# Optimization experiments

Measured on AMD Instinct MI355X. Metric: run time of the kernel, lower is better.

Reference implementation:

```python
import jax, jax.numpy as jnp
import numpy as np

EMBED = 768
HEADS = 12
HEAD_DIM = EMBED // HEADS  # 64
NUM_CLS = 1
WIN = 16        # one-sided window radius
DIL = 4         # dilation
THETA = 10000.0
COORD_HIGH = 100000.0


def _rotate_half(x):
    # [..., x1, x2, ...] -> [..., -x2, x1, ...] over adjacent pairs
    x1 = x[..., 0::2]
    x2 = x[..., 1::2]
    return jnp.stack([-x2, x1], axis=-1).reshape(x.shape)


def _rope2d(x, coords):
    # x: (B, H, L, head_dim); coords: (B, L, 2) pixel coords
    half = HEAD_DIM // 2
    inv_freq = 1.0 / THETA ** (jnp.arange(0, half, 2, dtype=jnp.float32) / half)  # (half/2,)
    xy = coords.astype(jnp.float32) / COORD_HIGH
    fx = xy[..., 0:1] * inv_freq  # (B, L, half/2)
    fy = xy[..., 1:2] * inv_freq
    fx = jnp.repeat(fx, 2, axis=-1)  # (B, L, half)
    fy = jnp.repeat(fy, 2, axis=-1)
    freqs = jnp.concatenate([fx, fy], axis=-1)  # (B, L, head_dim)
    cos = jnp.cos(freqs)[:, None]  # (B, 1, L, head_dim)
    sin = jnp.sin(freqs)[:, None]
    return x * cos + _rotate_half(x) * sin


def setup_inputs() -> dict:
    key = jax.random.key(0)
    ks = jax.random.split(key, 5)
    B, L = 1, 4096
    S = L + NUM_CLS
    x = jax.random.normal(ks[0], (B, S, EMBED), jnp.float32)
    coords = jax.random.randint(ks[1], (B, L, 2), 0, 100000).astype(jnp.int32)
    qkv_w = jax.random.normal(ks[2], (3 * EMBED, EMBED), jnp.float32) * 0.02
    qkv_b = jnp.zeros((3 * EMBED,), jnp.float32)
    out_w = jax.random.normal(ks[3], (EMBED, EMBED), jnp.float32) * 0.02
    out_b = jnp.zeros((EMBED,), jnp.float32)
    return {"x": x, "coords": coords, "qkv_w": qkv_w, "qkv_b": qkv_b,
            "out_w": out_w, "out_b": out_b}


def reference(x, coords, qkv_w, qkv_b, out_w, out_b):
    B, S, E = x.shape
    L = S - NUM_CLS
    # QKV projection -> (3, B, H, S, hd)
    qkv = (x @ qkv_w.T + qkv_b).reshape(B, S, 3, HEADS, HEAD_DIM)
    qkv = qkv.transpose(2, 0, 3, 1, 4)
    q, k, v = qkv[0], qkv[1], qkv[2]
    # 2D RoPE on patch tokens only
    q = jnp.concatenate([q[:, :, :NUM_CLS], _rope2d(q[:, :, NUM_CLS:], coords)], axis=2)
    k = jnp.concatenate([k[:, :, :NUM_CLS], _rope2d(k[:, :, NUM_CLS:], coords)], axis=2)
    scale = 1.0 / np.sqrt(HEAD_DIM).astype(np.float32)

    q_cls, k_cls, v_cls = q[:, :, :NUM_CLS], k[:, :, :NUM_CLS], v[:, :, :NUM_CLS]
    q_p, k_p, v_p = q[:, :, NUM_CLS:], k[:, :, NUM_CLS:], v[:, :, NUM_CLS:]

    # CLS (global) queries attend to everything
    cls_scores = jnp.einsum('bhqd,bhkd->bhqk', q_cls, k) * scale
    cls_out = jnp.einsum('bhqk,bhkd->bhqd', jax.nn.softmax(cls_scores, axis=-1), v)

    # Patch queries: single softmax over [CLS keys | dilated local window]
    win_len = 2 * WIN + 1
    pos = jnp.arange(L)
    rel = (jnp.arange(win_len) - WIN) * DIL
    key_idx = pos[:, None] + rel[None, :]          # (L, W) absolute patch key index
    valid = (key_idx >= 0) & (key_idx < L)         # boundary patches: masked, not wrapped
    gidx = jnp.clip(key_idx, 0, L - 1)
    k_win = jnp.take(k_p, gidx, axis=2)            # (B, H, L, W, hd)
    v_win = jnp.take(v_p, gidx, axis=2)
    s_win = jnp.einsum('bhld,bhlwd->bhlw', q_p, k_win) * scale
    s_win = jnp.where(valid[None, None], s_win, -jnp.inf)
    s_cls = jnp.einsum('bhld,bhcd->bhlc', q_p, k_cls) * scale
    attn = jax.nn.softmax(jnp.concatenate([s_cls, s_win], axis=-1), axis=-1)
    a_cls, a_win = attn[..., :NUM_CLS], attn[..., NUM_CLS:]
    patch_out = (jnp.einsum('bhlc,bhcd->bhld', a_cls, v_cls)
                 + jnp.einsum('bhlw,bhlwd->bhld', a_win, v_win))

    out = jnp.concatenate([cls_out, patch_out], axis=2)   # (B, H, S, hd)
    out = out.transpose(0, 2, 1, 3).reshape(B, S, E)
    return out @ out_w.T + out_b
```

## Files before the change

kernel.cpp:

```cpp
#include <hip/hip_runtime.h>
#include <hip/hip_bf16.h>

namespace {

constexpr int kS = 4097;
constexpr int kL = 4096;
constexpr int kE = 768;
constexpr int kH = 12;
constexpr int kD = 64;
constexpr int kQKVN = 2304;
constexpr int kT = 1024;
constexpr int kClsChunks = 32;
constexpr int kClsStride = 68;
constexpr float kScale = 0.125f;

typedef short short8 __attribute__((ext_vector_type(8)));
typedef short short4v __attribute__((ext_vector_type(4)));
typedef float f32x4 __attribute__((ext_vector_type(4)));

__device__ inline short f2bf(float x) {
  __hip_bfloat16 b = __float2bfloat16(x);
  return *reinterpret_cast<short*>(&b);
}
__device__ inline float bf2f(short u) {
  unsigned int x = ((unsigned int)(unsigned short)u) << 16;
  union { unsigned int u32; float f; } c;
  c.u32 = x;
  return c.f;
}

__device__ inline void store_c(float* p, float v) { *p = v; }
__device__ inline void store_c(short* p, float v) { *p = f2bf(v); }

__device__ inline int xcd_swz(int bid, int nwg) {
  const int q = nwg >> 3, r = nwg & 7;
  const int x = bid & 7, o = bid >> 3;
  return (x < r ? x * (q + 1) : r * (q + 1) + (x - r) * q) + o;
}

#define GLOAD_LDS16(g, l)                                                        \
  __builtin_amdgcn_global_load_lds(                                              \
      (const __attribute__((address_space(1))) unsigned int*)(g),                \
      (__attribute__((address_space(3))) unsigned int*)(l), 16, 0, 0)

__global__ __launch_bounds__(256) void cvt3_kernel(const float* __restrict__ x,
                                                   const float* __restrict__ w,
                                                   const float* __restrict__ ow,
                                                   short* __restrict__ xb,
                                                   short* __restrict__ wb,
                                                   short* __restrict__ owb,
                                                   int n4x, int n4w, int n4o) {
  const int total = n4x + n4w + n4o;
  int i = blockIdx.x * blockDim.x + threadIdx.x;
  const int stride = gridDim.x * blockDim.x;
  for (; i < total; i += stride) {
    const float* src;
    short* dst;
    int k;
    if (i < n4x) { src = x; dst = xb; k = i; }
    else if (i < n4x + n4w) { src = w; dst = wb; k = i - n4x; }
    else { src = ow; dst = owb; k = i - n4x - n4w; }
    f32x4 v = reinterpret_cast<const f32x4*>(src)[k];
    short4v o;
#pragma unroll
    for (int j = 0; j < 4; ++j) o[j] = f2bf(v[j]);
    reinterpret_cast<short4v*>(dst)[k] = o;
  }
}

template <bool ROPE, typename TC>
__global__ __launch_bounds__(256) void gemm_tile_kernel(const short* __restrict__ A,
                                                        const short* __restrict__ W,
                                                        const float* __restrict__ bias,
                                                        TC* __restrict__ C,
                                                        int Mreal, int N, int K, int ntm,
                                                        const int* __restrict__ coords) {
  __shared__ short Ash[2][64 * 32];
  __shared__ short Bsh[2][128 * 32];
  const int nwg = gridDim.x;
  const int wid = xcd_swz(blockIdx.x, nwg);
  const int m0 = (wid % ntm) * 64;
  const int n0 = (wid / ntm) * 128;
  const int t = threadIdx.x;
  const int lane = t & 63;
  const int wave = t >> 6;
  const int wr = wave >> 1, wc = wave & 1;
  const int lrow = lane & 15;
  const int kg = (lane >> 4) << 3;

  const int srow = t >> 2;
  const int scol = (t & 3) << 3;
  int arow = m0 + srow;        if (arow > Mreal - 1) arow = Mreal - 1;
  const int brow0 = n0 + srow;
  const int brow1 = n0 + 64 + srow;

  const short* pa = A + (size_t)arow * K + scol;
  const short* pb0 = W + (size_t)brow0 * K + scol;
  const short* pb1 = W + (size_t)brow1 * K + scol;

#define STAGE(buf, k0)                                  \
  do {                                                  \
    GLOAD_LDS16(pa + (k0), &Ash[buf][t * 8]);           \
    GLOAD_LDS16(pb0 + (k0), &Bsh[buf][t * 8]);          \
    GLOAD_LDS16(pb1 + (k0), &Bsh[buf][2048 + t * 8]);   \
  } while (0)

  f32x4 acc[2][4] = {};
  const int nsteps = K / 32;

  STAGE(0, 0);
  __syncthreads();

  int cur = 0;
  for (int tt = 0; tt < nsteps; ++tt) {
    if (tt + 1 < nsteps) STAGE(cur ^ 1, (tt + 1) * 32);

    short8 a[2], b[4];
#pragma unroll
    for (int mi = 0; mi < 2; ++mi)
      a[mi] = *reinterpret_cast<const short8*>(&Ash[cur][(wr * 32 + mi * 16 + lrow) * 32 + kg]);
#pragma unroll
    for (int ni = 0; ni < 4; ++ni)
      b[ni] = *reinterpret_cast<const short8*>(&Bsh[cur][(wc * 64 + ni * 16 + lrow) * 32 + kg]);
#pragma unroll
    for (int mi = 0; mi < 2; ++mi)
#pragma unroll
      for (int ni = 0; ni < 4; ++ni)
        acc[mi][ni] = __builtin_amdgcn_mfma_f32_16x16x32_bf16(a[mi], b[ni], acc[mi][ni], 0, 0, 0);

    __syncthreads();
    cur ^= 1;
  }
#undef STAGE

  const int rg = (lane >> 4) << 2;
  for (int ni = 0; ni < 4; ++ni) {
    const int col = n0 + wc * 64 + ni * 16 + lrow;
    const float bz = bias[col];
    const int sec = col / 768;
    const int dh = col & 63;
    const bool odd = dh & 1;
    const int jf = (dh >> 1) & 15;
    const bool usex = (dh >> 1) < 16;
    const float invf = __powf(10000.0f, -(float)jf * (1.0f / 16.0f));
    for (int mi = 0; mi < 2; ++mi) {
      const int rowb = m0 + wr * 32 + mi * 16 + rg;
#pragma unroll
      for (int r = 0; r < 4; ++r) {
        const int row = rowb + r;
        float v = acc[mi][ni][r] + bz;
        if (ROPE && sec != 2) {
          const float partner = __shfl_xor(v, 1);
          float cs = 1.f, sn = 0.f;
          if (row > 0) {
            const int cl = min(row, kS - 1) - 1;
            const float cx = (float)coords[cl * 2] * 1e-5f;
            const float cy = (float)coords[cl * 2 + 1] * 1e-5f;
            __sincosf((usex ? cx : cy) * invf, &sn, &cs);
          }
          v = odd ? (v * cs + partner * sn) : (v * cs - partner * sn);
          if (sec == 0) v *= kScale;
        }
        if (row < Mreal) store_c(&C[(size_t)row * N + col], v);
      }
    }
  }
}

__global__ __launch_bounds__(256) void attn_kernel(const short* __restrict__ qkv,
                                                   short* __restrict__ attn,
                                                   float* __restrict__ part) {
  __shared__ short Pl[4][32][104];
  __shared__ float sm[4], sl[4], sa[4][64];
  const int lane = threadIdx.x & 63;
  const int wv = threadIdx.x >> 6;

  if (blockIdx.x >= 384) {
    const int idx = blockIdx.x - 384;
    const int h = idx >> 5;
    const int c = idx & 31;
    const int start = c * 128;
    const int end = (c == kClsChunks - 1) ? kS : start + 128;
    const float qd = bf2f(qkv[h * kD + lane]);
    float m = -INFINITY, lsum = 0.f, acc = 0.f;
    for (int s = start + wv; s < end; s += 4) {
      float tt = qd * bf2f(qkv[(size_t)s * kQKVN + kE + h * kD + lane]);
      tt += __shfl_xor(tt, 1); tt += __shfl_xor(tt, 2); tt += __shfl_xor(tt, 4);
      tt += __shfl_xor(tt, 8); tt += __shfl_xor(tt, 16); tt += __shfl_xor(tt, 32);
      const float vd = bf2f(qkv[(size_t)s * kQKVN + 2 * kE + h * kD + lane]);
      const float mnew = fmaxf(m, tt);
      const float cor = __expf(m - mnew);
      const float p = __expf(tt - mnew);
      lsum = lsum * cor + p;
      acc = acc * cor + p * vd;
      m = mnew;
    }
    sa[wv][lane] = acc;
    if (lane == 0) { sm[wv] = m; sl[wv] = lsum; }
    __syncthreads();
    if (wv == 0) {
      float M = fmaxf(fmaxf(sm[0], sm[1]), fmaxf(sm[2], sm[3]));
      float Lt = 0.f, Av = 0.f;
#pragma unroll
      for (int w = 0; w < 4; ++w) {
        const float cw = __expf(sm[w] - M);
        Lt += sl[w] * cw;
        Av += sa[w][lane] * cw;
      }
      float* p = part + ((size_t)h * kClsChunks + c) * kClsStride;
      p[lane] = Av;
      if (lane == 0) { p[64] = M; p[65] = Lt; }
    }
    return;
  }

  const int unit = blockIdx.x * 4 + wv;
  const int t0 = (unit & 31) * 32;
  const int res = (unit >> 5) & 3;
  const int h = unit >> 7;
  const int lrow = lane & 15;
  const int lgrp = lane >> 4;
  const int kg = lgrp * 8;
  const int rg = lgrp * 4;

  f32x4 s_acc[2][4] = {};
  f32x4 s_cls[2] = {};
  short8 aq[2][2];
#pragma unroll
  for (int mi = 0; mi < 2; ++mi) {
    const int tq = t0 + mi * 16 + lrow;
    const size_t row = (size_t)(4 * tq + res + 1) * kQKVN + h * kD;
#pragma unroll
    for (int ks = 0; ks < 2; ++ks)
      aq[mi][ks] = *reinterpret_cast<const short8*>(qkv + row + ks * 32 + kg);
  }
#pragma unroll
  for (int ni = 0; ni < 4; ++ni) {
    int u = t0 - 16 + ni * 16 + lrow;
    u = min(max(u, 0), kT - 1);
    const size_t row = (size_t)(4 * u + res + 1) * kQKVN + kE + h * kD;
    short8 bk[2];
#pragma unroll
    for (int ks = 0; ks < 2; ++ks)
      bk[ks] = *reinterpret_cast<const short8*>(qkv + row + ks * 32 + kg);
#pragma unroll
    for (int mi = 0; mi < 2; ++mi)
#pragma unroll
      for (int ks = 0; ks < 2; ++ks)
        s_acc[mi][ni] = __builtin_amdgcn_mfma_f32_16x16x32_bf16(aq[mi][ks], bk[ks], s_acc[mi][ni], 0, 0, 0);
  }
  {
    short8 bc[2] = {};
    if (lrow == 0) {
#pragma unroll
      for (int ks = 0; ks < 2; ++ks)
        bc[ks] = *reinterpret_cast<const short8*>(qkv + kE + h * kD + ks * 32 + kg);
    }
#pragma unroll
    for (int mi = 0; mi < 2; ++mi)
#pragma unroll
      for (int ks = 0; ks < 2; ++ks)
        s_cls[mi] = __builtin_amdgcn_mfma_f32_16x16x32_bf16(aq[mi][ks], bc[ks], s_cls[mi], 0, 0, 0);
  }

#pragma unroll
  for (int i = 0; i < 2; ++i) {
    const int idx = i * 64 + lane;
    const int q = idx >> 2, ch = idx & 3;
    short8 z = {};
    *reinterpret_cast<short8*>(&Pl[wv][q][64 + ch * 8]) = z;
  }

#pragma unroll
  for (int mi = 0; mi < 2; ++mi) {
#pragma unroll
    for (int r = 0; r < 4; ++r) {
      const int q = mi * 16 + rg + r;
      float sw[4];
      float m = -INFINITY;
#pragma unroll
      for (int ni = 0; ni < 4; ++ni) {
        const int kk = ni * 16 + lrow;
        const int u = t0 - 16 + kk;
        const bool valid = (kk >= q) & (kk <= q + 32) & (u >= 0) & (u < kT);
        sw[ni] = valid ? s_acc[mi][ni][r] : -INFINITY;
        m = fmaxf(m, sw[ni]);
      }
      float scl = (lrow == 0) ? s_cls[mi][r] : -INFINITY;
      m = fmaxf(m, scl);
      m = fmaxf(m, __shfl_xor(m, 1)); m = fmaxf(m, __shfl_xor(m, 2));
      m = fmaxf(m, __shfl_xor(m, 4)); m = fmaxf(m, __shfl_xor(m, 8));
      float lsum = 0.f, ps[4];
#pragma unroll
      for (int ni = 0; ni < 4; ++ni) { ps[ni] = __expf(sw[ni] - m); lsum += ps[ni]; }
      const float pc = __expf(scl - m);
      lsum += pc;
      lsum += __shfl_xor(lsum, 1); lsum += __shfl_xor(lsum, 2);
      lsum += __shfl_xor(lsum, 4); lsum += __shfl_xor(lsum, 8);
      const float inv = __builtin_amdgcn_rcpf(lsum);
#pragma unroll
      for (int ni = 0; ni < 4; ++ni) Pl[wv][q][ni * 16 + lrow] = f2bf(ps[ni] * inv);
      if (lrow == 0) Pl[wv][q][64] = f2bf(pc * inv);
    }
  }

  f32x4 o_acc[4][2] = {};
#pragma unroll
  for (int ks = 0; ks < 3; ++ks) {
    short8 bp[2];
#pragma unroll
    for (int nq = 0; nq < 2; ++nq)
      bp[nq] = *reinterpret_cast<const short8*>(&Pl[wv][nq * 16 + lrow][ks * 32 + kg]);
    short8 av[4];
#pragma unroll
    for (int md = 0; md < 4; ++md) {
      if (ks < 2) {
        const int d = md * 16 + lrow;
#pragma unroll
        for (int e = 0; e < 8; ++e) {
          const int kk = ks * 32 + kg + e;
          int u = t0 - 16 + kk;
          u = min(max(u, 0), kT - 1);
          av[md][e] = qkv[(size_t)(4 * u + res + 1) * kQKVN + 2 * kE + h * kD + d];
        }
      } else {
        short8 z = {};
        av[md] = z;
        if (lgrp == 0)
          av[md][0] = qkv[2 * kE + h * kD + md * 16 + lrow];
      }
#pragma unroll
      for (int nq = 0; nq < 2; ++nq)
        o_acc[md][nq] = __builtin_amdgcn_mfma_f32_16x16x32_bf16(av[md], bp[nq], o_acc[md][nq], 0, 0, 0);
    }
  }

#pragma unroll
  for (int md = 0; md < 4; ++md)
#pragma unroll
    for (int nq = 0; nq < 2; ++nq)
#pragma unroll
      for (int r = 0; r < 4; ++r) {
        const int d = md * 16 + rg + r;
        const int q = nq * 16 + lrow;
        const int s = 4 * (t0 + q) + res + 1;
        attn[(size_t)s * kE + h * kD + d] = f2bf(o_acc[md][nq][r]);
      }
}

__global__ __launch_bounds__(64) void cls_combine_kernel(const float* __restrict__ part,
                                                         short* __restrict__ attn) {
  const int h = blockIdx.x;
  const int lane = threadIdx.x;
  float mc[kClsChunks], lc[kClsChunks], ac[kClsChunks];
#pragma unroll
  for (int c = 0; c < kClsChunks; ++c) {
    const float* p = part + ((size_t)h * kClsChunks + c) * kClsStride;
    mc[c] = p[64];
    lc[c] = p[65];
    ac[c] = p[lane];
  }
  float M = -INFINITY;
#pragma unroll
  for (int c = 0; c < kClsChunks; ++c) M = fmaxf(M, mc[c]);
  float L = 0.f, A = 0.f;
#pragma unroll
  for (int c = 0; c < kClsChunks; ++c) {
    const float w = __expf(mc[c] - M);
    L += lc[c] * w;
    A += ac[c] * w;
  }
  attn[h * kD + lane] = f2bf(A / L);
}

}

extern "C" void kernel_launch(void* const* d_in, const int* in_sizes, int n_in,
                              void* d_out, int out_size, void* d_ws, size_t ws_size,
                              hipStream_t stream) {
  const float* x = (const float*)d_in[0];
  const int* coords = (const int*)d_in[1];
  const float* qkv_w = (const float*)d_in[2];
  const float* qkv_b = (const float*)d_in[3];
  const float* out_w = (const float*)d_in[4];
  const float* out_b = (const float*)d_in[5];
  float* out = (float*)d_out;

  char* p = (char*)d_ws;
  short* qkvb = (short*)p;                p += (size_t)kS * kQKVN * sizeof(short);
  short* xb = (short*)p;                  p += (size_t)kS * kE * sizeof(short);
  short* wb = (short*)p;                  p += (size_t)kQKVN * kE * sizeof(short);
  short* owb = (short*)p;                 p += (size_t)kE * kE * sizeof(short);
  short* attnb = (short*)p;               p += (size_t)kS * kE * sizeof(short);
  float* clsp = (float*)p;

  const int n4x = kS * kE / 4;
  const int n4w = kQKVN * kE / 4;
  const int n4o = kE * kE / 4;
  cvt3_kernel<<<2048, 256, 0, stream>>>(x, qkv_w, out_w, xb, wb, owb, n4x, n4w, n4o);

  gemm_tile_kernel<true, short><<<1170, 256, 0, stream>>>(xb, wb, qkv_b, qkvb, kS, kQKVN, kE, 65, coords);
  attn_kernel<<<768, 256, 0, stream>>>(qkvb, attnb, clsp);
  cls_combine_kernel<<<kH, 64, 0, stream>>>(clsp, attnb);
  gemm_tile_kernel<false, float><<<390, 256, 0, stream>>>(attnb, owb, out_b, out, kS, kE, kE, 65, nullptr);
}
```

Baseline: 98.83 us.

## Double GEMM K-tile to 64 and XOR-swizzle LDS layout to avoid bank conflicts

The GEMM main loop now stages 64-wide K slices instead of 32, which halves the number of barrier-separated iterations. The LDS layout is XOR-swizzled by row so the 16-byte MFMA operand reads spread across banks instead of conflicting. LDS use per block doubles (about 48KB with double buffering), which may lower occupancy on the projection GEMMs.

New measurement: 95.67 us, median of 3. -3.2%, faster.

```diff
diff --git a/kernel.cpp b/kernel.cpp
--- a/kernel.cpp
+++ b/kernel.cpp
@@ -75,8 +75,8 @@
                                                         TC* __restrict__ C,
                                                         int Mreal, int N, int K, int ntm,
                                                         const int* __restrict__ coords) {
-  __shared__ short Ash[2][64 * 32];
-  __shared__ short Bsh[2][128 * 32];
+  __shared__ short Ash[2][64 * 64];
+  __shared__ short Bsh[2][128 * 64];
   const int nwg = gridDim.x;
   const int wid = xcd_swz(blockIdx.x, nwg);
   const int m0 = (wid % ntm) * 64;
@@ -86,54 +86,63 @@
   const int wave = t >> 6;
   const int wr = wave >> 1, wc = wave & 1;
   const int lrow = lane & 15;
-  const int kg = (lane >> 4) << 3;
-
-  const int srow = t >> 2;
-  const int scol = (t & 3) << 3;
-  int arow = m0 + srow;        if (arow > Mreal - 1) arow = Mreal - 1;
-  const int brow0 = n0 + srow;
-  const int brow1 = n0 + 64 + srow;
-
-  const short* pa = A + (size_t)arow * K + scol;
-  const short* pb0 = W + (size_t)brow0 * K + scol;
-  const short* pb1 = W + (size_t)brow1 * K + scol;
-
-#define STAGE(buf, k0)                                  \
-  do {                                                  \
-    GLOAD_LDS16(pa + (k0), &Ash[buf][t * 8]);           \
-    GLOAD_LDS16(pb0 + (k0), &Bsh[buf][t * 8]);          \
-    GLOAD_LDS16(pb1 + (k0), &Bsh[buf][2048 + t * 8]);   \
+  const int lgrp = lane >> 4;
+
+  const int srow = t >> 3;
+  const int scol = ((t & 7) ^ (srow & 7)) << 3;
+  int ar0 = m0 + srow;       if (ar0 > Mreal - 1) ar0 = Mreal - 1;
+  int ar1 = m0 + 32 + srow;  if (ar1 > Mreal - 1) ar1 = Mreal - 1;
+  const int br0 = n0 + srow, br1 = n0 + 32 + srow;
+  const int br2 = n0 + 64 + srow, br3 = n0 + 96 + srow;
+
+#define STAGE(buf, k0)                                                  \
+  do {                                                                  \
+    GLOAD_LDS16(A + (size_t)ar0 * K + (k0) + scol, &Ash[buf][t * 8]);   \
+    GLOAD_LDS16(A + (size_t)ar1 * K + (k0) + scol, &Ash[buf][2048 + t * 8]); \
+    GLOAD_LDS16(W + (size_t)br0 * K + (k0) + scol, &Bsh[buf][t * 8]);   \
+    GLOAD_LDS16(W + (size_t)br1 * K + (k0) + scol, &Bsh[buf][2048 + t * 8]); \
+    GLOAD_LDS16(W + (size_t)br2 * K + (k0) + scol, &Bsh[buf][4096 + t * 8]); \
+    GLOAD_LDS16(W + (size_t)br3 * K + (k0) + scol, &Bsh[buf][6144 + t * 8]); \
   } while (0)
 
   f32x4 acc[2][4] = {};
-  const int nsteps = K / 32;
+  const int nsteps = K / 64;
 
   STAGE(0, 0);
   __syncthreads();
 
   int cur = 0;
   for (int tt = 0; tt < nsteps; ++tt) {
-    if (tt + 1 < nsteps) STAGE(cur ^ 1, (tt + 1) * 32);
-
-    short8 a[2], b[4];
-#pragma unroll
-    for (int mi = 0; mi < 2; ++mi)
-      a[mi] = *reinterpret_cast<const short8*>(&Ash[cur][(wr * 32 + mi * 16 + lrow) * 32 + kg]);
-#pragma unroll
-    for (int ni = 0; ni < 4; ++ni)
-      b[ni] = *reinterpret_cast<const short8*>(&Bsh[cur][(wc * 64 + ni * 16 + lrow) * 32 + kg]);
-#pragma unroll
-    for (int mi = 0; mi < 2; ++mi)
-#pragma unroll
-      for (int ni = 0; ni < 4; ++ni)
-        acc[mi][ni] = __builtin_amdgcn_mfma_f32_16x16x32_bf16(a[mi], b[ni], acc[mi][ni], 0, 0, 0);
+    if (tt + 1 < nsteps) STAGE(cur ^ 1, (tt + 1) * 64);
+
+#pragma unroll
+    for (int ks = 0; ks < 2; ++ks) {
+      short8 a[2], b[4];
+#pragma unroll
+      for (int mi = 0; mi < 2; ++mi) {
+        const int row = wr * 32 + mi * 16 + lrow;
+        const int ch = (ks * 4 + lgrp) ^ (row & 7);
+        a[mi] = *reinterpret_cast<const short8*>(&Ash[cur][row * 64 + ch * 8]);
+      }
+#pragma unroll
+      for (int ni = 0; ni < 4; ++ni) {
+        const int row = wc * 64 + ni * 16 + lrow;
+        const int ch = (ks * 4 + lgrp) ^ (row & 7);
+        b[ni] = *reinterpret_cast<const short8*>(&Bsh[cur][row * 64 + ch * 8]);
+      }
+#pragma unroll
+      for (int mi = 0; mi < 2; ++mi)
+#pragma unroll
+        for (int ni = 0; ni < 4; ++ni)
+          acc[mi][ni] = __builtin_amdgcn_mfma_f32_16x16x32_bf16(a[mi], b[ni], acc[mi][ni], 0, 0, 0);
+    }
 
     __syncthreads();
     cur ^= 1;
   }
 #undef STAGE
 
-  const int rg = (lane >> 4) << 2;
+  const int rg = lgrp << 2;
   for (int ni = 0; ni < 4; ++ni) {
     const int col = n0 + wc * 64 + ni * 16 + lrow;
     const float bz = bias[col];
```

## Restructure GEMMs to keep full-K weight slab in LDS and stream A from registers

Applied to the files above, without the earlier changes.

Replaces the double-buffered 64x128 K-stepped GEMM with a kernel that loads a whole 64x768 weight slab into LDS once, using an XOR swizzle against bank conflicts. A is read straight from global memory into registers with a three-deep software pipeline, so the K loop has no barriers. Each 512-thread block covers 512 rows, giving 324 and 108 blocks instead of 1170 and 390. This removes per-step synchronisation and LDS staging of A, at the cost of 96KB of LDS per block (low occupancy), a grid smaller than the CU count for the output projection, and uncoalesced global loads of A.

After: 149.5 us. 51.3% more time.

```diff
diff --git a/kernel.cpp b/kernel.cpp
--- a/kernel.cpp
+++ b/kernel.cpp
@@ -69,73 +69,82 @@
 }
 
 template <bool ROPE, typename TC>
-__global__ __launch_bounds__(256) void gemm_tile_kernel(const short* __restrict__ A,
+__global__ __launch_bounds__(512) void gemm_flat_kernel(const short* __restrict__ A,
                                                         const short* __restrict__ W,
                                                         const float* __restrict__ bias,
                                                         TC* __restrict__ C,
-                                                        int Mreal, int N, int K, int ntm,
+                                                        int Mreal, int N, int nn,
                                                         const int* __restrict__ coords) {
-  __shared__ short Ash[2][64 * 32];
-  __shared__ short Bsh[2][128 * 32];
+  __shared__ short Wsh[64 * 768];
   const int nwg = gridDim.x;
   const int wid = xcd_swz(blockIdx.x, nwg);
-  const int m0 = (wid % ntm) * 64;
-  const int n0 = (wid / ntm) * 128;
+  const int n0 = (wid % nn) * 64;
+  const int m0 = (wid / nn) * 512;
   const int t = threadIdx.x;
   const int lane = t & 63;
   const int wave = t >> 6;
-  const int wr = wave >> 1, wc = wave & 1;
   const int lrow = lane & 15;
-  const int kg = (lane >> 4) << 3;
-
-  const int srow = t >> 2;
-  const int scol = (t & 3) << 3;
-  int arow = m0 + srow;        if (arow > Mreal - 1) arow = Mreal - 1;
-  const int brow0 = n0 + srow;
-  const int brow1 = n0 + 64 + srow;
-
-  const short* pa = A + (size_t)arow * K + scol;
-  const short* pb0 = W + (size_t)brow0 * K + scol;
-  const short* pb1 = W + (size_t)brow1 * K + scol;
-
-#define STAGE(buf, k0)                                  \
-  do {                                                  \
-    GLOAD_LDS16(pa + (k0), &Ash[buf][t * 8]);           \
-    GLOAD_LDS16(pb0 + (k0), &Bsh[buf][t * 8]);          \
-    GLOAD_LDS16(pb1 + (k0), &Bsh[buf][2048 + t * 8]);   \
+  const int lgrp = lane >> 4;
+  const int kg = lgrp * 8;
+
+#pragma unroll
+  for (int j = 0; j < 12; ++j) {
+    const int c = j * 512 + t;
+    const int row = c / 96;
+    const int ch = c % 96;
+    GLOAD_LDS16(W + (size_t)(n0 + row) * 768 + (ch ^ (row & 7)) * 8, &Wsh[c * 8]);
+  }
+
+  const short* pa[4];
+#pragma unroll
+  for (int mi = 0; mi < 4; ++mi) {
+    int r = m0 + wave * 64 + mi * 16 + lrow;
+    if (r > Mreal - 1) r = Mreal - 1;
+    pa[mi] = A + (size_t)r * 768 + kg;
+  }
+
+#define LOADA(st, s)                                                   \
+  do {                                                                 \
+    _Pragma("unroll") for (int mi = 0; mi < 4; ++mi)                   \
+        st[mi] = *reinterpret_cast<const short8*>(pa[mi] + (s) * 32);  \
   } while (0)
 
-  f32x4 acc[2][4] = {};
-  const int nsteps = K / 32;
-
-  STAGE(0, 0);
+#define COMPUTE(st, s)                                                             \
+  do {                                                                             \
+    short8 b[4];                                                                   \
+    const int cb = (s) * 4;                                                        \
+    _Pragma("unroll") for (int ni = 0; ni < 4; ++ni) {                             \
+      const int row = ni * 16 + lrow;                                              \
+      const int ch = (cb + lgrp) ^ (row & 7);                                      \
+      b[ni] = *reinterpret_cast<const short8*>(&Wsh[row * 768 + ch * 8]);          \
+    }                                                                              \
+    _Pragma("unroll") for (int mi = 0; mi < 4; ++mi)                               \
+        _Pragma("unroll") for (int ni = 0; ni < 4; ++ni)                           \
+            acc[mi][ni] =                                                          \
+                __builtin_amdgcn_mfma_f32_16x16x32_bf16(st[mi], b[ni], acc[mi][ni], 0, 0, 0); \
+  } while (0)
+
+  f32x4 acc[4][4] = {};
+  short8 ua[4], va[4], wa[4];
+  LOADA(ua, 0);
+  LOADA(va, 1);
+  LOADA(wa, 2);
   __syncthreads();
 
-  int cur = 0;
-  for (int tt = 0; tt < nsteps; ++tt) {
-    if (tt + 1 < nsteps) STAGE(cur ^ 1, (tt + 1) * 32);
-
-    short8 a[2], b[4];
-#pragma unroll
-    for (int mi = 0; mi < 2; ++mi)
-      a[mi] = *reinterpret_cast<const short8*>(&Ash[cur][(wr * 32 + mi * 16 + lrow) * 32 + kg]);
-#pragma unroll
-    for (int ni = 0; ni < 4; ++ni)
-      b[ni] = *reinterpret_cast<const short8*>(&Bsh[cur][(wc * 64 + ni * 16 + lrow) * 32 + kg]);
-#pragma unroll
-    for (int mi = 0; mi < 2; ++mi)
-#pragma unroll
-      for (int ni = 0; ni < 4; ++ni)
-        acc[mi][ni] = __builtin_amdgcn_mfma_f32_16x16x32_bf16(a[mi], b[ni], acc[mi][ni], 0, 0, 0);
-
-    __syncthreads();
-    cur ^= 1;
-  }
-#undef STAGE
-
-  const int rg = (lane >> 4) << 2;
+  for (int tt = 0; tt < 24; tt += 3) {
+    COMPUTE(ua, tt);
+    if (tt + 3 < 24) LOADA(ua, tt + 3);
+    COMPUTE(va, tt + 1);
+    if (tt + 4 < 24) LOADA(va, tt + 4);
+    COMPUTE(wa, tt + 2);
+    if (tt + 5 < 24) LOADA(wa, tt + 5);
+  }
+#undef LOADA
+#undef COMPUTE
+
+  const int rg = lgrp << 2;
   for (int ni = 0; ni < 4; ++ni) {
-    const int col = n0 + wc * 64 + ni * 16 + lrow;
+    const int col = n0 + ni * 16 + lrow;
     const float bz = bias[col];
     const int sec = col / 768;
     const int dh = col & 63;
@@ -143,8 +152,8 @@
     const int jf = (dh >> 1) & 15;
     const bool usex = (dh >> 1) < 16;
     const float invf = __powf(10000.0f, -(float)jf * (1.0f / 16.0f));
-    for (int mi = 0; mi < 2; ++mi) {
-      const int rowb = m0 + wr * 32 + mi * 16 + rg;
+    for (int mi = 0; mi < 4; ++mi) {
+      const int rowb = m0 + wave * 64 + mi * 16 + rg;
 #pragma unroll
       for (int r = 0; r < 4; ++r) {
         const int row = rowb + r;
@@ -399,8 +408,8 @@
   const int n4o = kE * kE / 4;
   cvt3_kernel<<<2048, 256, 0, stream>>>(x, qkv_w, out_w, xb, wb, owb, n4x, n4w, n4o);
 
-  gemm_tile_kernel<true, short><<<1170, 256, 0, stream>>>(xb, wb, qkv_b, qkvb, kS, kQKVN, kE, 65, coords);
+  gemm_flat_kernel<true, short><<<324, 512, 0, stream>>>(xb, wb, qkv_b, qkvb, kS, kQKVN, 36, coords);
   attn_kernel<<<768, 256, 0, stream>>>(qkvb, attnb, clsp);
   cls_combine_kernel<<<kH, 64, 0, stream>>>(clsp, attnb);
-  gemm_tile_kernel<false, float><<<390, 256, 0, stream>>>(attnb, owb, out_b, out, kS, kE, kE, 65, nullptr);
-}
+  gemm_flat_kernel<false, float><<<108, 512, 0, stream>>>(attnb, owb, out_b, out, kS, kE, 12, nullptr);
+}
```

## Replace direct global-to-LDS loads with register-staged prefetch two steps ahead

Applied to the files above, without the earlier changes.

The GEMM main loop no longer uses global_load_lds into a double-buffered LDS tile. It now loads tiles into registers two k-steps ahead (two register sets ping-ponged), writes them to LDS after compute, and syncs with an explicit lgkmcnt wait and s_barrier. The aim is to hide global memory latency better by deepening the prefetch. The cost is more VGPRs and extra LDS write instructions. The loop also assumes an even number of k-steps.

Result: slower. 103.8 us (+5.0%).

```diff
diff --git a/kernel.cpp b/kernel.cpp
--- a/kernel.cpp
+++ b/kernel.cpp
@@ -37,11 +37,6 @@
   const int x = bid & 7, o = bid >> 3;
   return (x < r ? x * (q + 1) : r * (q + 1) + (x - r) * q) + o;
 }
-
-#define GLOAD_LDS16(g, l)                                                        \
-  __builtin_amdgcn_global_load_lds(                                              \
-      (const __attribute__((address_space(1))) unsigned int*)(g),                \
-      (__attribute__((address_space(3))) unsigned int*)(l), 16, 0, 0)
 
 __global__ __launch_bounds__(256) void cvt3_kernel(const float* __restrict__ x,
                                                    const float* __restrict__ w,
@@ -98,40 +93,70 @@
   const short* pb0 = W + (size_t)brow0 * K + scol;
   const short* pb1 = W + (size_t)brow1 * K + scol;
 
-#define STAGE(buf, k0)                                  \
-  do {                                                  \
-    GLOAD_LDS16(pa + (k0), &Ash[buf][t * 8]);           \
-    GLOAD_LDS16(pb0 + (k0), &Bsh[buf][t * 8]);          \
-    GLOAD_LDS16(pb1 + (k0), &Bsh[buf][2048 + t * 8]);   \
+#define LOADSET(Sa, Sb0, Sb1, k)                            \
+  do {                                                      \
+    Sa = *reinterpret_cast<const short8*>(pa + (k));        \
+    Sb0 = *reinterpret_cast<const short8*>(pb0 + (k));      \
+    Sb1 = *reinterpret_cast<const short8*>(pb1 + (k));      \
+  } while (0)
+
+#define WRITESET(Sa, Sb0, Sb1, buf)                         \
+  do {                                                      \
+    *reinterpret_cast<short8*>(&Ash[buf][t * 8]) = Sa;      \
+    *reinterpret_cast<short8*>(&Bsh[buf][t * 8]) = Sb0;     \
+    *reinterpret_cast<short8*>(&Bsh[buf][2048 + t * 8]) = Sb1; \
+  } while (0)
+
+#define COMPUTE(buf)                                                                   \
+  do {                                                                                 \
+    short8 a[2], b[4];                                                                 \
+    _Pragma("unroll") for (int mi = 0; mi < 2; ++mi)                                   \
+        a[mi] = *reinterpret_cast<const short8*>(                                      \
+            &Ash[buf][(wr * 32 + mi * 16 + lrow) * 32 + kg]);                          \
+    _Pragma("unroll") for (int ni = 0; ni < 4; ++ni)                                   \
+        b[ni] = *reinterpret_cast<const short8*>(                                      \
+            &Bsh[buf][(wc * 64 + ni * 16 + lrow) * 32 + kg]);                          \
+    _Pragma("unroll") for (int mi = 0; mi < 2; ++mi)                                   \
+        _Pragma("unroll") for (int ni = 0; ni < 4; ++ni)                               \
+            acc[mi][ni] =                                                              \
+                __builtin_amdgcn_mfma_f32_16x16x32_bf16(a[mi], b[ni], acc[mi][ni], 0, 0, 0); \
+  } while (0)
+
+#define ENDSTEP                                             \
+  do {                                                      \
+    asm volatile("s_waitcnt lgkmcnt(0)" ::: "memory");      \
+    __builtin_amdgcn_sched_barrier(0);                      \
+    __builtin_amdgcn_s_barrier();                           \
+    __builtin_amdgcn_sched_barrier(0);                      \
   } while (0)
 
   f32x4 acc[2][4] = {};
   const int nsteps = K / 32;
 
-  STAGE(0, 0);
-  __syncthreads();
+  short8 Pa, Pb0, Pb1, Qa, Qb0, Qb1;
+  LOADSET(Pa, Pb0, Pb1, 0);
+  WRITESET(Pa, Pb0, Pb1, 0);
+  LOADSET(Pa, Pb0, Pb1, 32);
+  LOADSET(Qa, Qb0, Qb1, 64);
+  ENDSTEP;
 
   int cur = 0;
-  for (int tt = 0; tt < nsteps; ++tt) {
-    if (tt + 1 < nsteps) STAGE(cur ^ 1, (tt + 1) * 32);
-
-    short8 a[2], b[4];
-#pragma unroll
-    for (int mi = 0; mi < 2; ++mi)
-      a[mi] = *reinterpret_cast<const short8*>(&Ash[cur][(wr * 32 + mi * 16 + lrow) * 32 + kg]);
-#pragma unroll
-    for (int ni = 0; ni < 4; ++ni)
-      b[ni] = *reinterpret_cast<const short8*>(&Bsh[cur][(wc * 64 + ni * 16 + lrow) * 32 + kg]);
-#pragma unroll
-    for (int mi = 0; mi < 2; ++mi)
-#pragma unroll
-      for (int ni = 0; ni < 4; ++ni)
-        acc[mi][ni] = __builtin_amdgcn_mfma_f32_16x16x32_bf16(a[mi], b[ni], acc[mi][ni], 0, 0, 0);
-
-    __syncthreads();
+  for (int tt = 0; tt < nsteps; tt += 2) {
+    COMPUTE(cur);
+    if (tt + 1 < nsteps) WRITESET(Pa, Pb0, Pb1, cur ^ 1);
+    if (tt + 3 < nsteps) LOADSET(Pa, Pb0, Pb1, (tt + 3) * 32);
+    ENDSTEP;
     cur ^= 1;
-  }
-#undef STAGE
+    COMPUTE(cur);
+    if (tt + 2 < nsteps) WRITESET(Qa, Qb0, Qb1, cur ^ 1);
+    if (tt + 4 < nsteps) LOADSET(Qa, Qb0, Qb1, (tt + 4) * 32);
+    ENDSTEP;
+    cur ^= 1;
+  }
+#undef LOADSET
+#undef WRITESET
+#undef COMPUTE
+#undef ENDSTEP
 
   const int rg = (lane >> 4) << 2;
   for (int ni = 0; ni < 4; ++ni) {
```
